# Kernel tuning notes

Measured on AMD Instinct MI355X. Metric: run time of the kernel, lower is better.

The kernel has to match this reference:

```python
import jax, jax.numpy as jnp
import numpy as np

MIN_DIST = 32  # minimum_extrema_distance from init_kwargs


def _extrema_mask(x):
    # x: [L]. Matches torch: dx padded with 0 on right (>0) and left (<=0);
    # sign = (1 - sign(x)).bool() is True iff x <= 0.
    dx = x[1:] - x[:-1]
    right = jnp.pad(dx, (0, 1)) > 0        # rising on the right
    left = jnp.pad(dx, (1, 0)) <= 0        # non-rising on the left
    neg = x <= 0
    valleys = right & left & neg
    peaks = (~right) & (~left) & (~neg)
    return valleys | peaks


def _suppress(x):
    # Greedy NMS-like suppression over one sample. x: [L]
    L = x.shape[0]
    e = _extrema_mask(x)
    # Sort ALL positions by |x| descending, with non-extrema pushed to the end
    key = jnp.where(e, jnp.abs(x), -jnp.inf)
    order = jnp.argsort(-key)              # candidate j -> original index order[j]
    valid = e[order]                       # which sorted candidates are real extrema
    idx = order                            # original positions, in sorted order

    def step(sec, i):
        # If candidate i not yet suppressed: suppress all candidates within
        # MIN_DIST of its position, then un-suppress itself.
        cond = jnp.logical_not(sec[i])
        window = (idx >= idx[i] - MIN_DIST) & (idx <= idx[i] + MIN_DIST)
        new_sec = jnp.where(cond, (sec | window).at[i].set(False), sec)
        return new_sec, None

    sec0 = jnp.logical_not(valid)          # non-extrema start suppressed
    sec, _ = jax.lax.scan(step, sec0, jnp.arange(L))
    primary_sorted = valid & jnp.logical_not(sec)
    # scatter back to original positions (order is a permutation)
    primary = jnp.zeros((L,), dtype=bool).at[order].set(primary_sorted)
    return jnp.where(primary, x, jnp.zeros_like(x))


def setup_inputs() -> dict:
    key = jax.random.key(0)
    input_ = jax.random.normal(key, (128, 1, 4096), dtype=jnp.float32)
    return {"input_": input_}


def reference(input_):
    x = input_[:, 0, :]                    # [B, L]
    out = jax.vmap(_suppress)(x)           # [B, L]
    return out[:, None, :]                 # [B, 1, L]
```

## Files before the change

kernel.cpp:

```cpp
#include <hip/hip_runtime.h>

#define L 4096
#define NT 256
#define C 16
#define NC (NT + 4)
#define SS 20

typedef unsigned int u32;
typedef unsigned long long u64;

static __device__ __forceinline__ u32 umax(u32 a, u32 b) { return a > b ? a : b; }

__global__ __launch_bounds__(NT) void extrema_nms_kernel(const float* __restrict__ in,
                                                         float* __restrict__ out) {
    __shared__ u32 pfxS[NC * SS];
    __shared__ u32 sfxS[NC * SS];
    __shared__ u32 winmF[2 * NC];
    __shared__ int flagsF[2];

    const int tid = threadIdx.x;
    const int cc = tid + 2;
    const int base = tid * C;
    const float* xrow = in + (size_t)blockIdx.x * L;

    if (tid < 4 * SS) {
        int rsel = tid / SS;
        int row = (rsel & 1) + ((rsel >> 1) ? (NT + 2) : 0);
        int col = tid % SS;
        pfxS[row * SS + col] = 0;
        sfxS[row * SS + col] = 0;
    }
    if (tid < 4) {
        int slot = (tid & 1) + ((tid >> 1) ? (NT + 2) : 0);
        winmF[slot] = 0;
        winmF[NC + slot] = 0;
    }
    if (tid == 0) { flagsF[0] = 0; flagsF[1] = 0; }

    float xv[C];
    #pragma unroll
    for (int k = 0; k < C; k += 4) {
        float4 f = *reinterpret_cast<const float4*>(xrow + base + k);
        xv[k] = f.x; xv[k + 1] = f.y; xv[k + 2] = f.z; xv[k + 3] = f.w;
    }
    float xl = (base > 0) ? xrow[base - 1] : 0.0f;
    float xr = (base + C < L) ? xrow[base + C] : 0.0f;

    u32 key[C];
    #pragma unroll
    for (int o = 0; o < C; ++o) {
        int i = base + o;
        float xi = xv[o];
        float xp = (o == 0) ? xl : xv[o - 1];
        float xn = (o == C - 1) ? xr : xv[o + 1];
        bool right = (i < L - 1) && (xn > xi);
        bool left  = (i == 0) || (xi <= xp);
        bool neg   = (xi <= 0.0f);
        bool ext = (right && left && neg) || (!right && !left && !neg);
        key[o] = ext ? ((__float_as_uint(xi) & 0x7fffffffu) + 1u) : 0u;
    }

    u32 run, om;
    {
        u32 pf[C], sf[C];
        u32 p = 0, nom = 0;
        #pragma unroll
        for (int o = 0; o < C; ++o) { u32 k = key[o]; if (k > p) { p = k; nom = (u32)o; } pf[o] = p; }
        u32 s = 0;
        #pragma unroll
        for (int o = C - 1; o >= 0; --o) { s = umax(s, key[o]); sf[o] = s; }
        u32* pr = &pfxS[cc * SS];
        u32* sr = &sfxS[cc * SS];
        #pragma unroll
        for (int k4 = 0; k4 < C; k4 += 4) {
            *reinterpret_cast<uint4*>(pr + k4) = make_uint4(pf[k4], pf[k4+1], pf[k4+2], pf[k4+3]);
            *reinterpret_cast<uint4*>(sr + k4) = make_uint4(sf[k4], sf[k4+1], sf[k4+2], sf[k4+3]);
        }
        pr[16] = p;
        run = p; om = nom;
    }
    u32 keptm = 0;
    __syncthreads();

    for (int r = 0; r < 200; ++r) {
        u32 wm = 0;
        if (run) {
            u32 bL = umax(sfxS[(cc - 2) * SS + om], pfxS[(cc - 1) * SS + 16]);
            u32 bR = umax(pfxS[(cc + 1) * SS + 16], pfxS[(cc + 2) * SS + om]);
            if (bL < run && bR <= run) wm = 1u << om;
        }
        winmF[(r & 1) * NC + cc] = wm;
        if (wm) { keptm |= wm; flagsF[r & 1] = 1; }
        __syncthreads();

        int go = flagsF[r & 1];
        u32 m0 = 0, m1 = 0, m3 = 0, m4 = 0;
        if (run) {
            const int pp = (r & 1) * NC;
            m0 = winmF[pp + cc - 2]; m1 = winmF[pp + cc - 1];
            m3 = winmF[pp + cc + 1]; m4 = winmF[pp + cc + 2];
        }
        if (tid == 0) flagsF[(r + 1) & 1] = 0;
        if (!go) break;
        u64 W0 = (u64)m0 | ((u64)m1 << 16) | ((u64)wm << 32) | ((u64)m3 << 48);
        u32 W1 = m4;
        u32 supmask = 0;
        if (W0) { int h0 = 63 - __clzll(W0); supmask = (h0 >= 15) ? 0xffffu : ((2u << h0) - 1u); }
        if (W1) { int l1 = __ffs((int)W1) - 1; supmask |= ~((1u << l1) - 1u); }
        supmask &= 0xffffu;
        if (run && supmask) {
            #pragma unroll
            for (int o = 0; o < C; ++o) key[o] = ((supmask >> o) & 1u) ? 0u : key[o];
            u32 pf[C], sf[C];
            u32 p = 0, nom = 0;
            #pragma unroll
            for (int o = 0; o < C; ++o) { u32 k = key[o]; if (k > p) { p = k; nom = (u32)o; } pf[o] = p; }
            u32 s = 0;
            #pragma unroll
            for (int o = C - 1; o >= 0; --o) { s = umax(s, key[o]); sf[o] = s; }
            u32* pr = &pfxS[cc * SS];
            u32* sr = &sfxS[cc * SS];
            #pragma unroll
            for (int k4 = 0; k4 < C; k4 += 4) {
                *reinterpret_cast<uint4*>(pr + k4) = make_uint4(pf[k4], pf[k4+1], pf[k4+2], pf[k4+3]);
                *reinterpret_cast<uint4*>(sr + k4) = make_uint4(sf[k4], sf[k4+1], sf[k4+2], sf[k4+3]);
            }
            pr[16] = p;
            run = p; om = nom;
        }
        __syncthreads();
    }

    float* orow = out + (size_t)blockIdx.x * L;
    #pragma unroll
    for (int k = 0; k < C; k += 4) {
        float4 f;
        f.x = ((keptm >> (k + 0)) & 1u) ? xv[k + 0] : 0.0f;
        f.y = ((keptm >> (k + 1)) & 1u) ? xv[k + 1] : 0.0f;
        f.z = ((keptm >> (k + 2)) & 1u) ? xv[k + 2] : 0.0f;
        f.w = ((keptm >> (k + 3)) & 1u) ? xv[k + 3] : 0.0f;
        *reinterpret_cast<float4*>(orow + base + k) = f;
    }
}

extern "C" void kernel_launch(void* const* d_in, const int* in_sizes, int n_in,
                              void* d_out, int out_size, void* d_ws, size_t ws_size,
                              hipStream_t stream) {
    const float* in = (const float*)d_in[0];
    float* out = (float*)d_out;
    int rows = in_sizes[0] / L;
    extrema_nms_kernel<<<rows, NT, 0, stream>>>(in, out);
}
```

Baseline: 11.79 us.

## Run multiple relaxed NMS sub-steps per barrier with change-driven termination

```diff
diff --git a/kernel.cpp b/kernel.cpp
--- a/kernel.cpp
+++ b/kernel.cpp
@@ -5,18 +5,62 @@
 #define C 16
 #define NC (NT + 4)
 #define SS 20
+#define KSUB 2
 
 typedef unsigned int u32;
 typedef unsigned long long u64;
 
 static __device__ __forceinline__ u32 umax(u32 a, u32 b) { return a > b ? a : b; }
 
+
+#define RESCAN()                                                         \
+    do {                                                                 \
+        u32 pf_[C], sf_[C];                                              \
+        u32 p_ = 0, nom_ = 0;                                            \
+        _Pragma("unroll")                                                \
+        for (int o_ = 0; o_ < C; ++o_) {                                 \
+            u32 k_ = key[o_];                                            \
+            if (k_ > p_) { p_ = k_; nom_ = (u32)o_; }                    \
+            pf_[o_] = p_;                                                \
+        }                                                                \
+        u32 s_ = 0;                                                      \
+        _Pragma("unroll")                                                \
+        for (int o_ = C - 1; o_ >= 0; --o_) {                            \
+            s_ = umax(s_, key[o_]); sf_[o_] = s_;                        \
+        }                                                                \
+        u32* pr_ = &pfxS[cc * SS];                                       \
+        u32* sr_ = &sfxS[cc * SS];                                       \
+        _Pragma("unroll")                                                \
+        for (int q_ = 0; q_ < C; q_ += 4) {                              \
+            *reinterpret_cast<uint4*>(pr_ + q_) =                        \
+                make_uint4(pf_[q_], pf_[q_+1], pf_[q_+2], pf_[q_+3]);    \
+            *reinterpret_cast<uint4*>(sr_ + q_) =                        \
+                make_uint4(sf_[q_], sf_[q_+1], sf_[q_+2], sf_[q_+3]);    \
+        }                                                                \
+        TAc[cc] = p_;                                                    \
+        run = p_; om = nom_;                                             \
+    } while (0)
+
+#define ZERO_SCANS()                                                     \
+    do {                                                                 \
+        uint4 z_ = make_uint4(0, 0, 0, 0);                               \
+        u32* pr_ = &pfxS[cc * SS];                                       \
+        u32* sr_ = &sfxS[cc * SS];                                       \
+        _Pragma("unroll")                                                \
+        for (int q_ = 0; q_ < C; q_ += 4) {                              \
+            *reinterpret_cast<uint4*>(pr_ + q_) = z_;                    \
+            *reinterpret_cast<uint4*>(sr_ + q_) = z_;                    \
+        }                                                                \
+        TAc[cc] = 0;                                                     \
+    } while (0)
+
 __global__ __launch_bounds__(NT) void extrema_nms_kernel(const float* __restrict__ in,
                                                          float* __restrict__ out) {
     __shared__ u32 pfxS[NC * SS];
     __shared__ u32 sfxS[NC * SS];
-    __shared__ u32 winmF[2 * NC];
-    __shared__ int flagsF[2];
+    __shared__ u32 TAc[NC];
+    __shared__ u32 winC[NC];
+    __shared__ u32 lastChange;
 
     const int tid = threadIdx.x;
     const int cc = tid + 2;
@@ -32,10 +76,11 @@
     }
     if (tid < 4) {
         int slot = (tid & 1) + ((tid >> 1) ? (NT + 2) : 0);
-        winmF[slot] = 0;
-        winmF[NC + slot] = 0;
+        TAc[slot] = 0;
+        winC[slot] = 0;
     }
-    if (tid == 0) { flagsF[0] = 0; flagsF[1] = 0; }
+    winC[cc] = 0;
+    if (tid == 0) lastChange = 0;
 
     float xv[C];
     #pragma unroll
@@ -60,75 +105,75 @@
         key[o] = ext ? ((__float_as_uint(xi) & 0x7fffffffu) + 1u) : 0u;
     }
 
+    u32 alivem = 0;
+    #pragma unroll
+    for (int o = 0; o < C; ++o) if (key[o]) alivem |= (1u << o);
     u32 run, om;
-    {
-        u32 pf[C], sf[C];
-        u32 p = 0, nom = 0;
-        #pragma unroll
-        for (int o = 0; o < C; ++o) { u32 k = key[o]; if (k > p) { p = k; nom = (u32)o; } pf[o] = p; }
-        u32 s = 0;
-        #pragma unroll
-        for (int o = C - 1; o >= 0; --o) { s = umax(s, key[o]); sf[o] = s; }
-        u32* pr = &pfxS[cc * SS];
-        u32* sr = &sfxS[cc * SS];
-        #pragma unroll
-        for (int k4 = 0; k4 < C; k4 += 4) {
-            *reinterpret_cast<uint4*>(pr + k4) = make_uint4(pf[k4], pf[k4+1], pf[k4+2], pf[k4+3]);
-            *reinterpret_cast<uint4*>(sr + k4) = make_uint4(sf[k4], sf[k4+1], sf[k4+2], sf[k4+3]);
-        }
-        pr[16] = p;
-        run = p; om = nom;
-    }
+    RESCAN();
     u32 keptm = 0;
+    u64 appliedW0 = 0;
+    u32 appliedW1 = 0;
     __syncthreads();
 
-    for (int r = 0; r < 200; ++r) {
-        u32 wm = 0;
-        if (run) {
-            u32 bL = umax(sfxS[(cc - 2) * SS + om], pfxS[(cc - 1) * SS + 16]);
-            u32 bR = umax(pfxS[(cc + 1) * SS + 16], pfxS[(cc + 2) * SS + om]);
-            if (bL < run && bR <= run) wm = 1u << om;
+    for (int r = 1; r <= 200; ++r) {
+        bool changedAny = false;
+        #pragma unroll
+        for (int s = 0; s < KSUB; ++s) {
+            if (run) {
+                u32 m0 = winC[cc - 2], m1 = winC[cc - 1];
+                u32 m3 = winC[cc + 1], m4 = winC[cc + 2];
+                u32 sL = sfxS[(cc - 2) * SS + om];
+                u32 tL = TAc[cc - 1];
+                u32 tR = TAc[cc + 1];
+                u32 pR = pfxS[(cc + 2) * SS + om];
+
+                u64 W0 = (u64)m0 | ((u64)m1 << 16) | ((u64)m3 << 48);
+                u32 W1 = m4;
+                bool omChanged = false;
+                if ((W0 ^ appliedW0) | (u64)(W1 ^ appliedW1)) {
+                    appliedW0 = W0; appliedW1 = W1;
+                    u32 supmask = 0;
+                    if (W0) { int h0 = 63 - __clzll(W0);
+                              supmask = (h0 >= 15) ? 0xffffu : ((2u << h0) - 1u); }
+                    if (W1) { int l1 = __ffs((int)W1) - 1;
+                              supmask |= ~((1u << l1) - 1u); }
+                    u32 nA = alivem & ~supmask;
+                    if (nA != alivem) {
+                        alivem = nA;
+                        changedAny = true;
+                        if (nA == 0) {
+                            ZERO_SCANS();
+                            run = 0;
+                        } else {
+                            #pragma unroll
+                            for (int o = 0; o < C; ++o)
+                                key[o] = ((supmask >> o) & 1u) ? 0u : key[o];
+                            RESCAN();
+                            omChanged = true;
+                        }
+                    }
+                }
+
+                if (run) {
+                    if (omChanged) {
+                        sL = sfxS[(cc - 2) * SS + om];
+                        pR = pfxS[(cc + 2) * SS + om];
+                    }
+                    u32 bL = umax(sL, tL);
+                    u32 bR = umax(tR, pR);
+                    if (bL < run && bR <= run) {
+                        keptm |= 1u << om;
+                        winC[cc] = 1u << om;
+                        changedAny = true;
+                        ZERO_SCANS();
+                        run = 0; alivem = 0;
+                    }
+                }
+            }
         }
-        winmF[(r & 1) * NC + cc] = wm;
-        if (wm) { keptm |= wm; flagsF[r & 1] = 1; }
+        if (changedAny) lastChange = r;
         __syncthreads();
-
-        int go = flagsF[r & 1];
-        u32 m0 = 0, m1 = 0, m3 = 0, m4 = 0;
-        if (run) {
-            const int pp = (r & 1) * NC;
-            m0 = winmF[pp + cc - 2]; m1 = winmF[pp + cc - 1];
-            m3 = winmF[pp + cc + 1]; m4 = winmF[pp + cc + 2];
-        }
-        if (tid == 0) flagsF[(r + 1) & 1] = 0;
-        if (!go) break;
-        u64 W0 = (u64)m0 | ((u64)m1 << 16) | ((u64)wm << 32) | ((u64)m3 << 48);
-        u32 W1 = m4;
-        u32 supmask = 0;
-        if (W0) { int h0 = 63 - __clzll(W0); supmask = (h0 >= 15) ? 0xffffu : ((2u << h0) - 1u); }
-        if (W1) { int l1 = __ffs((int)W1) - 1; supmask |= ~((1u << l1) - 1u); }
-        supmask &= 0xffffu;
-        if (run && supmask) {
-            #pragma unroll
-            for (int o = 0; o < C; ++o) key[o] = ((supmask >> o) & 1u) ? 0u : key[o];
-            u32 pf[C], sf[C];
-            u32 p = 0, nom = 0;
-            #pragma unroll
-            for (int o = 0; o < C; ++o) { u32 k = key[o]; if (k > p) { p = k; nom = (u32)o; } pf[o] = p; }
-            u32 s = 0;
-            #pragma unroll
-            for (int o = C - 1; o >= 0; --o) { s = umax(s, key[o]); sf[o] = s; }
-            u32* pr = &pfxS[cc * SS];
-            u32* sr = &sfxS[cc * SS];
-            #pragma unroll
-            for (int k4 = 0; k4 < C; k4 += 4) {
-                *reinterpret_cast<uint4*>(pr + k4) = make_uint4(pf[k4], pf[k4+1], pf[k4+2], pf[k4+3]);
-                *reinterpret_cast<uint4*>(sr + k4) = make_uint4(sf[k4], sf[k4+1], sf[k4+2], sf[k4+3]);
-            }
-            pr[16] = p;
-            run = p; om = nom;
-        }
-        __syncthreads();
+        if (lastChange < (u32)r) break;
     }
 
     float* orow = out + (size_t)blockIdx.x * L;
```

Result: slower. 14.32 us (+21.5%).

## Widen per-thread chunks to 32 elements and simplify neighbor suppression logic

Applied to the files above, without the earlier changes.

```diff
diff --git a/kernel.cpp b/kernel.cpp
--- a/kernel.cpp
+++ b/kernel.cpp
@@ -1,145 +1,167 @@
 #include <hip/hip_runtime.h>
 
 #define L 4096
-#define NT 256
-#define C 16
-#define NC (NT + 4)
-#define SS 20
+#define NT 128
+#define C 32
+#define NCC (NT + 2)
+#define SS 36
+#define MAXR 256
 
 typedef unsigned int u32;
-typedef unsigned long long u64;
 
 static __device__ __forceinline__ u32 umax(u32 a, u32 b) { return a > b ? a : b; }
 
+
+#define SCANS_OUT()                                                       \
+    do {                                                                  \
+        u32* pr_ = &pfxS[cc * SS];                                        \
+        u32* sr_ = &sfxS[cc * SS];                                        \
+        u32 p_ = 0, nom_ = 0;                                             \
+        _Pragma("unroll")                                                 \
+        for (int g_ = 0; g_ < C; g_ += 4) {                               \
+            u32 t0_, t1_, t2_, t3_;                                       \
+            u32 k_;                                                       \
+            k_ = key[g_ + 0]; if (k_ > p_) { p_ = k_; nom_ = g_ + 0; } t0_ = p_; \
+            k_ = key[g_ + 1]; if (k_ > p_) { p_ = k_; nom_ = g_ + 1; } t1_ = p_; \
+            k_ = key[g_ + 2]; if (k_ > p_) { p_ = k_; nom_ = g_ + 2; } t2_ = p_; \
+            k_ = key[g_ + 3]; if (k_ > p_) { p_ = k_; nom_ = g_ + 3; } t3_ = p_; \
+            *reinterpret_cast<uint4*>(pr_ + g_) = make_uint4(t0_, t1_, t2_, t3_); \
+        }                                                                 \
+        u32 s_ = 0;                                                       \
+        _Pragma("unroll")                                                 \
+        for (int g_ = C - 4; g_ >= 0; g_ -= 4) {                          \
+            u32 t3_ = umax(s_, key[g_ + 3]);                              \
+            u32 t2_ = umax(t3_, key[g_ + 2]);                             \
+            u32 t1_ = umax(t2_, key[g_ + 1]);                             \
+            u32 t0_ = umax(t1_, key[g_ + 0]);                             \
+            *reinterpret_cast<uint4*>(sr_ + g_) = make_uint4(t0_, t1_, t2_, t3_); \
+            s_ = t0_;                                                     \
+        }                                                                 \
+        run = p_; om = nom_;                                              \
+    } while (0)
+
 __global__ __launch_bounds__(NT) void extrema_nms_kernel(const float* __restrict__ in,
                                                          float* __restrict__ out) {
-    __shared__ u32 pfxS[NC * SS];
-    __shared__ u32 sfxS[NC * SS];
-    __shared__ u32 winmF[2 * NC];
+    __shared__ u32 pfxS[NCC * SS];
+    __shared__ u32 sfxS[NCC * SS];
+    __shared__ u32 winmF[2 * NCC];
     __shared__ int flagsF[2];
 
     const int tid = threadIdx.x;
-    const int cc = tid + 2;
+    const int cc = tid + 1;
     const int base = tid * C;
     const float* xrow = in + (size_t)blockIdx.x * L;
 
-    if (tid < 4 * SS) {
-        int rsel = tid / SS;
-        int row = (rsel & 1) + ((rsel >> 1) ? (NT + 2) : 0);
+    if (tid < 2 * SS) {
+        int row = (tid < SS) ? 0 : (NCC - 1);
         int col = tid % SS;
         pfxS[row * SS + col] = 0;
         sfxS[row * SS + col] = 0;
     }
     if (tid < 4) {
-        int slot = (tid & 1) + ((tid >> 1) ? (NT + 2) : 0);
+        int slot = ((tid & 1) ? (NCC - 1) : 0) + ((tid >> 1) ? NCC : 0);
         winmF[slot] = 0;
-        winmF[NC + slot] = 0;
     }
     if (tid == 0) { flagsF[0] = 0; flagsF[1] = 0; }
 
-    float xv[C];
-    #pragma unroll
-    for (int k = 0; k < C; k += 4) {
-        float4 f = *reinterpret_cast<const float4*>(xrow + base + k);
-        xv[k] = f.x; xv[k + 1] = f.y; xv[k + 2] = f.z; xv[k + 3] = f.w;
-    }
-    float xl = (base > 0) ? xrow[base - 1] : 0.0f;
-    float xr = (base + C < L) ? xrow[base + C] : 0.0f;
-
     u32 key[C];
-    #pragma unroll
-    for (int o = 0; o < C; ++o) {
-        int i = base + o;
-        float xi = xv[o];
-        float xp = (o == 0) ? xl : xv[o - 1];
-        float xn = (o == C - 1) ? xr : xv[o + 1];
-        bool right = (i < L - 1) && (xn > xi);
-        bool left  = (i == 0) || (xi <= xp);
-        bool neg   = (xi <= 0.0f);
-        bool ext = (right && left && neg) || (!right && !left && !neg);
-        key[o] = ext ? ((__float_as_uint(xi) & 0x7fffffffu) + 1u) : 0u;
+    {
+        float xm1 = (tid > 0) ? xrow[base - 1] : 0.0f;
+        float xpC = (base + C < L) ? xrow[base + C] : 0.0f;
+        float4 cur = *reinterpret_cast<const float4*>(xrow + base);
+        float prev = xm1;
+        #pragma unroll
+        for (int g = 0; g < C / 4; ++g) {
+            float4 nxt;
+            if (g < C / 4 - 1) nxt = *reinterpret_cast<const float4*>(xrow + base + 4 * (g + 1));
+            else nxt = make_float4(xpC, 0.f, 0.f, 0.f);
+            float e0 = cur.x, e1 = cur.y, e2 = cur.z, e3 = cur.w;
+            float pv[4] = {prev, e0, e1, e2};
+            float cv[4] = {e0, e1, e2, e3};
+            float nv[4] = {e1, e2, e3, nxt.x};
+            #pragma unroll
+            for (int j = 0; j < 4; ++j) {
+                int i = base + 4 * g + j;
+                float xi = cv[j];
+                bool right = (i < L - 1) && (nv[j] > xi);
+                bool left  = (i == 0) || (xi <= pv[j]);
+                bool neg   = (xi <= 0.0f);
+                bool ext = (right && left && neg) || (!right && !left && !neg);
+                key[4 * g + j] = ext ? ((__float_as_uint(xi) & 0x7fffffffu) + 1u) : 0u;
+            }
+            prev = e3; cur = nxt;
+        }
     }
 
+    u32 alivem = 0;
+    #pragma unroll
+    for (int o = 0; o < C; ++o) if (key[o]) alivem |= (1u << o);
     u32 run, om;
-    {
-        u32 pf[C], sf[C];
-        u32 p = 0, nom = 0;
-        #pragma unroll
-        for (int o = 0; o < C; ++o) { u32 k = key[o]; if (k > p) { p = k; nom = (u32)o; } pf[o] = p; }
-        u32 s = 0;
-        #pragma unroll
-        for (int o = C - 1; o >= 0; --o) { s = umax(s, key[o]); sf[o] = s; }
-        u32* pr = &pfxS[cc * SS];
-        u32* sr = &sfxS[cc * SS];
-        #pragma unroll
-        for (int k4 = 0; k4 < C; k4 += 4) {
-            *reinterpret_cast<uint4*>(pr + k4) = make_uint4(pf[k4], pf[k4+1], pf[k4+2], pf[k4+3]);
-            *reinterpret_cast<uint4*>(sr + k4) = make_uint4(sf[k4], sf[k4+1], sf[k4+2], sf[k4+3]);
-        }
-        pr[16] = p;
-        run = p; om = nom;
-    }
+    SCANS_OUT();
     u32 keptm = 0;
     __syncthreads();
 
-    for (int r = 0; r < 200; ++r) {
+    for (int r = 0; r < MAXR; ++r) {
         u32 wm = 0;
         if (run) {
-            u32 bL = umax(sfxS[(cc - 2) * SS + om], pfxS[(cc - 1) * SS + 16]);
-            u32 bR = umax(pfxS[(cc + 1) * SS + 16], pfxS[(cc + 2) * SS + om]);
+            u32 bL = sfxS[(cc - 1) * SS + om];
+            u32 bR = pfxS[(cc + 1) * SS + om];
             if (bL < run && bR <= run) wm = 1u << om;
         }
-        winmF[(r & 1) * NC + cc] = wm;
+        winmF[(r & 1) * NCC + cc] = wm;
         if (wm) { keptm |= wm; flagsF[r & 1] = 1; }
         __syncthreads();
 
         int go = flagsF[r & 1];
-        u32 m0 = 0, m1 = 0, m3 = 0, m4 = 0;
+        u32 mL = 0, mR = 0;
         if (run) {
-            const int pp = (r & 1) * NC;
-            m0 = winmF[pp + cc - 2]; m1 = winmF[pp + cc - 1];
-            m3 = winmF[pp + cc + 1]; m4 = winmF[pp + cc + 2];
+            const int pp = (r & 1) * NCC;
+            mL = winmF[pp + cc - 1];
+            mR = winmF[pp + cc + 1];
         }
         if (tid == 0) flagsF[(r + 1) & 1] = 0;
         if (!go) break;
-        u64 W0 = (u64)m0 | ((u64)m1 << 16) | ((u64)wm << 32) | ((u64)m3 << 48);
-        u32 W1 = m4;
-        u32 supmask = 0;
-        if (W0) { int h0 = 63 - __clzll(W0); supmask = (h0 >= 15) ? 0xffffu : ((2u << h0) - 1u); }
-        if (W1) { int l1 = __ffs((int)W1) - 1; supmask |= ~((1u << l1) - 1u); }
-        supmask &= 0xffffu;
-        if (run && supmask) {
-            #pragma unroll
-            for (int o = 0; o < C; ++o) key[o] = ((supmask >> o) & 1u) ? 0u : key[o];
-            u32 pf[C], sf[C];
-            u32 p = 0, nom = 0;
-            #pragma unroll
-            for (int o = 0; o < C; ++o) { u32 k = key[o]; if (k > p) { p = k; nom = (u32)o; } pf[o] = p; }
-            u32 s = 0;
-            #pragma unroll
-            for (int o = C - 1; o >= 0; --o) { s = umax(s, key[o]); sf[o] = s; }
-            u32* pr = &pfxS[cc * SS];
-            u32* sr = &sfxS[cc * SS];
-            #pragma unroll
-            for (int k4 = 0; k4 < C; k4 += 4) {
-                *reinterpret_cast<uint4*>(pr + k4) = make_uint4(pf[k4], pf[k4+1], pf[k4+2], pf[k4+3]);
-                *reinterpret_cast<uint4*>(sr + k4) = make_uint4(sf[k4], sf[k4+1], sf[k4+2], sf[k4+3]);
+        if (run) {
+            u32 supmask = 0;
+            if (wm) {
+                supmask = 0xffffffffu;
+            } else {
+                if (mL) { int q = __ffs((int)mL) - 1; supmask |= (2u << q) - 1u; }
+                if (mR) { int q = __ffs((int)mR) - 1; supmask |= ~((1u << q) - 1u); }
             }
-            pr[16] = p;
-            run = p; om = nom;
+            u32 nA = alivem & ~supmask;
+            if (nA != alivem) {
+                alivem = nA;
+                if (nA == 0) {
+                    uint4 z = make_uint4(0, 0, 0, 0);
+                    u32* pr = &pfxS[cc * SS];
+                    u32* sr = &sfxS[cc * SS];
+                    #pragma unroll
+                    for (int q4 = 0; q4 < C; q4 += 4) {
+                        *reinterpret_cast<uint4*>(pr + q4) = z;
+                        *reinterpret_cast<uint4*>(sr + q4) = z;
+                    }
+                    run = 0;
+                } else {
+                    #pragma unroll
+                    for (int o = 0; o < C; ++o)
+                        key[o] = ((supmask >> o) & 1u) ? 0u : key[o];
+                    SCANS_OUT();
+                }
+            }
         }
         __syncthreads();
     }
 
     float* orow = out + (size_t)blockIdx.x * L;
     #pragma unroll
-    for (int k = 0; k < C; k += 4) {
-        float4 f;
-        f.x = ((keptm >> (k + 0)) & 1u) ? xv[k + 0] : 0.0f;
-        f.y = ((keptm >> (k + 1)) & 1u) ? xv[k + 1] : 0.0f;
-        f.z = ((keptm >> (k + 2)) & 1u) ? xv[k + 2] : 0.0f;
-        f.w = ((keptm >> (k + 3)) & 1u) ? xv[k + 3] : 0.0f;
-        *reinterpret_cast<float4*>(orow + base + k) = f;
+    for (int g = 0; g < C / 4; ++g) {
+        float4 f = *reinterpret_cast<const float4*>(xrow + base + 4 * g);
+        f.x = ((keptm >> (4 * g + 0)) & 1u) ? f.x : 0.0f;
+        f.y = ((keptm >> (4 * g + 1)) & 1u) ? f.y : 0.0f;
+        f.z = ((keptm >> (4 * g + 2)) & 1u) ? f.z : 0.0f;
+        f.w = ((keptm >> (4 * g + 3)) & 1u) ? f.w : 0.0f;
+        *reinterpret_cast<float4*>(orow + base + 4 * g) = f;
     }
 }
 
```

Result: slower. 15.03 us (+27.5%).
